# Kernel optimization log

Measured on AMD Instinct MI355X. Metric: run time of the kernel, lower is better.

Reference implementation:

```python
import jax, jax.numpy as jnp
import numpy as np

B, T, H, L, V = 256, 20, 512, 2, 8964
LQ, LH, LI = 40, 80, 49
BETA = 3.0


def setup_inputs() -> dict:
    key = jax.random.key(0)
    ks = iter(jax.random.split(key, 40))
    s = 1.0 / np.sqrt(H)
    n = lambda shape, sc=s: jax.random.normal(next(ks), shape, jnp.float32) * sc
    inp = {
        'emb': n((B, T, H), 1.0),
        'question': n((B, LQ, 2 * H), 1.0),
        'history': n((B, LH, 2 * H), 1.0),
        'image': n((B, LI, 2 * H), 1.0),
        'h0': jnp.zeros((L, B, H), jnp.float32),
        'c0': jnp.zeros((L, B, H), jnp.float32),
        # LSTM params (both layers have input dim H since ninp == nhid)
        'Wih': n((L, 4 * H, H)), 'Whh': n((L, 4 * H, H)),
        'bih': jnp.zeros((L, 4 * H), jnp.float32), 'bhh': jnp.zeros((L, 4 * H), jnp.float32),
        # question attention: w_q (2H->H), ans_q (H->H), Wa_q (H->1)
        'Wq': n((H, 2 * H)), 'bq': jnp.zeros((H,), jnp.float32),
        'Wansq': n((H, H)), 'bansq': jnp.zeros((H,), jnp.float32),
        'waq': n((1, H)), 'baq': jnp.zeros((1,), jnp.float32),
        # history attention
        'Wh': n((H, 2 * H)), 'bh': jnp.zeros((H,), jnp.float32),
        'Wansh': n((H, H)), 'bansh': jnp.zeros((H,), jnp.float32),
        'wah': n((1, H)), 'bah': jnp.zeros((1,), jnp.float32),
        # image attention
        'Wi': n((H, 2 * H)), 'bi': jnp.zeros((H,), jnp.float32),
        'Wansi': n((H, H)), 'bansi': jnp.zeros((H,), jnp.float32),
        'wai': n((1, H)), 'bai': jnp.zeros((1,), jnp.float32),
        # concat fusion (3H -> H)
        'Wcat': n((H, 3 * H)), 'bcat': jnp.zeros((H,), jnp.float32),
        # decoder SimpleClassifier: 2H -> 4H -> V
        'Wd1': n((4 * H, 2 * H)), 'bd1': jnp.zeros((4 * H,), jnp.float32),
        'Wd2': n((V, 4 * H), 1.0 / np.sqrt(4 * H)), 'bd2': jnp.zeros((V,), jnp.float32),
    }
    return inp


def reference(emb, question, history, image, h0, c0,
              Wih, Whh, bih, bhh,
              Wq, bq, Wansq, bansq, waq, baq,
              Wh, bh, Wansh, bansh, wah, bah,
              Wi, bi, Wansi, bansi, wai, bai,
              Wcat, bcat, Wd1, bd1, Wd2, bd2):
    nlayers = Wih.shape[0]
    # context projections are timestep-invariant: hoist out of the loop
    q_emb = question @ Wq.T + bq   # [B, LQ, H]
    h_emb = history @ Wh.T + bh    # [B, LH, H]
    i_emb = image @ Wi.T + bi      # [B, LI, H]

    def attend(ctx, out, Wans, bans, wa, ba):
        # ctx: [B, Lx, H], out: [B, H]
        a = jnp.tanh(ctx + (out @ Wans.T + bans)[:, None, :])
        logits = jnp.einsum('blh,h->bl', a, wa[0]) + ba[0]
        w = jax.nn.softmax(logits, axis=1)
        return jnp.einsum('bl,blh->bh', w, ctx)

    def step(carry, x_t):
        h, c = carry  # each [L, B, H]
        inp = x_t
        hs, cs = [], []
        for l in range(nlayers):
            gates = inp @ Wih[l].T + h[l] @ Whh[l].T + bih[l] + bhh[l]
            gi, gf, gg, go = jnp.split(gates, 4, axis=-1)  # torch gate order i,f,g,o
            cn = jax.nn.sigmoid(gf) * c[l] + jax.nn.sigmoid(gi) * jnp.tanh(gg)
            hn = jax.nn.sigmoid(go) * jnp.tanh(cn)
            hs.append(hn); cs.append(cn)
            inp = hn
        out = inp  # top-layer output [B, H]
        fq = attend(q_emb, out, Wansq, bansq, waq, baq)
        fh = attend(h_emb, out, Wansh, bansh, wah, bah)
        fi = attend(i_emb, out, Wansi, bansi, wai, bai)
        cat = jnp.tanh(jnp.concatenate([fq, fh, fi], axis=1) @ Wcat.T + bcat)
        fusion = jnp.concatenate([out, cat], axis=1)  # [B, 2H]
        dec = jax.nn.relu(fusion @ Wd1.T + bd1) @ Wd2.T + bd2
        lp = jax.nn.log_softmax(BETA * dec, axis=1)
        return (jnp.stack(hs), jnp.stack(cs)), lp

    (hT, cT), lps = jax.lax.scan(step, (h0, c0), jnp.swapaxes(emb, 0, 1))
    return jnp.swapaxes(lps, 0, 1), hT, cT
```

## Files before the change

### kernel.cpp

```cpp
#include <hip/hip_runtime.h>
#include <cmath>

#define B_ 256
#define T_ 20
#define H_ 512
#define V_ 8964
#define LQ_ 40
#define LH_ 80
#define LI_ 49
#define BT_ (B_ * T_)
#define BH_ (B_ * H_)
#define NPAD_ 9216
#define BETA_ 3.0f

#define MEGA_LSTM_ 128
#define MEGA_CTXQ_ 320
#define MEGA_CTXH_ 640
#define MEGA_CTXI_ 392
#define MEGA_CTX_ (MEGA_CTXQ_ + MEGA_CTXH_ + MEGA_CTXI_)
#define MEGA_GRID_ (MEGA_LSTM_ + MEGA_CTX_)

#define PREP_WCVT_ 2560
#define PREP_WD2_  9216
#define PREP_EMB_  1280
#define PREP_PERM_ 2048
#define PREP_H0_   128
#define PREP_BIAS_ 2
#define PREP_GRID_ (PREP_WCVT_ + PREP_WD2_ + PREP_EMB_ + PREP_PERM_ + PREP_H0_ + PREP_BIAS_)

typedef __attribute__((ext_vector_type(8))) short bf16x8;
typedef __attribute__((ext_vector_type(4))) float f32x4;
typedef __attribute__((ext_vector_type(8))) unsigned short u16x8;

static __device__ __forceinline__ unsigned short f2bf(float f) {
    union { float f; unsigned u; } v; v.f = f;
    unsigned r = v.u + 0x7FFF + ((v.u >> 16) & 1);
    return (unsigned short)(r >> 16);
}
static __device__ __forceinline__ float bf2f(unsigned short u) {
    union { unsigned u; float f; } v; v.u = ((unsigned)u) << 16;
    return v.f;
}
static __device__ __forceinline__ float fast_tanh(float x) {
    const float e = __expf(2.f * x);
    return 1.f - 2.f * __builtin_amdgcn_rcpf(e + 1.f);
}
static __device__ __forceinline__ float fast_sigmoid(float x) {
    return __builtin_amdgcn_rcpf(1.f + __expf(-x));
}
static __device__ __forceinline__ void st16_sc(unsigned short* p, unsigned short v) {
    unsigned int vv = v;
    asm volatile("global_store_short %0, %1, off sc0 sc1" :: "v"(p), "v"(vv) : "memory");
}
static __device__ __forceinline__ int ld32_sc(const int* p) {
    int v;
    asm volatile("global_load_dword %0, %1, off sc0 sc1\n\t"
                 "s_waitcnt vmcnt(0)"
                 : "=v"(v) : "v"(p) : "memory");
    return v;
}
#define GLD16(g, l) __builtin_amdgcn_global_load_lds(                                   \
    (const __attribute__((address_space(1))) unsigned int*)(unsigned long long)(const void*)(g), \
    (__attribute__((address_space(3))) unsigned int*)(unsigned int)(unsigned long long)(void*)(l), \
    16, 0, 0)

static __device__ __forceinline__ u16x8 cvt8(const float* p)
{
    float4 a = *reinterpret_cast<const float4*>(p);
    float4 b = *reinterpret_cast<const float4*>(p + 4);
    u16x8 v;
    v[0] = f2bf(a.x); v[1] = f2bf(a.y); v[2] = f2bf(a.z); v[3] = f2bf(a.w);
    v[4] = f2bf(b.x); v[5] = f2bf(b.y); v[6] = f2bf(b.z); v[7] = f2bf(b.w);
    return v;
}

struct PrepArgs {
    const float* wsrc[8]; unsigned short* wdst[8];
    const float* Wd2; unsigned short* Wd2p;
    const float* emb; unsigned short* emb_bf;
    const float* psrc[4]; unsigned short* pdst[4];
    const float* h0; unsigned short* hbuf;
    const float* bih; const float* bhh; float* bp0; float* bp1;
};

__global__ __launch_bounds__(256) void prep_kernel(PrepArgs a)
{
    static constexpr long long WSZ[8] = {524288, 524288, 524288, 262144,
                                         262144, 262144, 786432, 2097152};
    int g = blockIdx.x;
    const int tid = threadIdx.x;

    if (g < PREP_WCVT_) {
        long long off = (long long)g * 2048;
        int seg = 0;
#pragma unroll
        for (int i = 0; i < 8; ++i)
            if (seg == i && off >= WSZ[i]) { off -= WSZ[i]; ++seg; }
        const long long e = off + (long long)tid * 8;
        *reinterpret_cast<u16x8*>(a.wdst[seg] + e) = cvt8(a.wsrc[seg] + e);
        return;
    }
    g -= PREP_WCVT_;
    if (g < PREP_WD2_) {
        const long long e = (long long)g * 2048 + tid * 8;
        const long long row = e >> 11;
        u16x8 v;
        if (row < V_) v = cvt8(a.Wd2 + e);
        else v = (u16x8)0;
        *reinterpret_cast<u16x8*>(a.Wd2p + e) = v;
        return;
    }
    g -= PREP_WD2_;
    if (g < PREP_EMB_) {
        const long long e = (long long)g * 2048 + tid * 8;
        *reinterpret_cast<u16x8*>(a.emb_bf + e) = cvt8(a.emb + e);
        return;
    }
    g -= PREP_EMB_;
    if (g < PREP_PERM_) {
        const int which = g >> 9;
        const long long e0 = ((long long)(g & 511) * 256 + tid) * 8;
        const int drow = (int)(e0 >> 9);
        const int col = (int)(e0 & 511);
        const int gg = (drow >> 4) & 3;
        const int hsrc = ((drow >> 6) << 4) | (drow & 15);
        const int srow = (gg << 9) | hsrc;
        *reinterpret_cast<u16x8*>(a.pdst[which] + e0) =
            cvt8(a.psrc[which] + (long long)srow * 512 + col);
        return;
    }
    g -= PREP_PERM_;
    if (g < PREP_H0_) {
        const int half = g >> 6;
        const long long e = (long long)(g & 63) * 2048 + tid * 8;
        unsigned short* dst = a.hbuf + (half ? 4LL * BH_ : 0LL);
        *reinterpret_cast<u16x8*>(dst + e) = cvt8(a.h0 + (long long)half * BH_ + e);
        return;
    }
    g -= PREP_H0_;
    {
        const float* b1 = g ? a.bih + 2048 : a.bih;
        const float* b2 = g ? a.bhh + 2048 : a.bhh;
        float* dst = g ? a.bp1 : a.bp0;
#pragma unroll
        for (int i = 0; i < 8; ++i) {
            const int n = i * 256 + tid;
            const int gg = (n >> 4) & 3;
            const int h = ((n >> 6) << 4) | (n & 15);
            const int orig = (gg << 9) | h;
            dst[n] = b1[orig] + b2[orig];
        }
    }
}

static __device__ __forceinline__ int4 ldA8f(const float* A, long long idx)
{
    union { int4 i4; u16x8 v; } r;
    r.v = cvt8(A + idx);
    return r.i4;
}

template <int ACT, int OUTBF, int AF32>
__global__ __launch_bounds__(256, 2) void mfma_gemm(
    const void* __restrict__ A, const unsigned short* __restrict__ W,
    const float* __restrict__ bias1, const float* __restrict__ bias2,
    void* __restrict__ C, long long ldc, int Nreal, int K)
{
    __shared__ __align__(16) unsigned short As[2][128][32];
    __shared__ __align__(16) unsigned short Bs[2][128][32];
    const int tid = threadIdx.x;
    const int lane = tid & 63;
    const int wave = tid >> 6;
    const int wm = wave >> 1, wn = wave & 1;

    const int nwg = gridDim.x * gridDim.y;
    const int orig = blockIdx.y * gridDim.x + blockIdx.x;
    const int xcd = orig & 7, base = orig >> 3;
    const int q8 = nwg >> 3, r8 = nwg & 7;
    const int wg = (xcd < r8 ? xcd * (q8 + 1) : r8 * (q8 + 1) + (xcd - r8) * q8) + base;

    int MI = 8192 / (K << AF32);
    if (MI < 1) MI = 1;
    if (MI > (int)gridDim.y) MI = gridDim.y;
    const int slabSz = gridDim.x * MI;
    const int fullSlabs = gridDim.y / MI;
    const int fullRegion = fullSlabs * slabSz;
    int m0, n0;
    if (wg < fullRegion) {
        const int mb = wg / slabSz, rem = wg % slabSz;
        m0 = (mb * MI + rem % MI) * 128;
        n0 = (rem / MI) * 128;
    } else {
        const int rem = wg - fullRegion;
        const int TM = gridDim.y - fullSlabs * MI;
        m0 = (fullSlabs * MI + rem % TM) * 128;
        n0 = (rem / TM) * 128;
    }

    const int r = tid >> 2;
    const int ck = (tid & 3) * 8;

    const unsigned short* Wp = W + (long long)n0 * K;

    f32x4 acc[4][4] = {};
    int cur = 0;

    if constexpr (!AF32) {
        const unsigned short* Ab = (const unsigned short*)A;
        auto issue = [&](int k0, int buf) {
            const unsigned short* ga0 = Ab + (long long)(m0 + r) * K + k0 + ck;
            const unsigned short* ga1 = Ab + (long long)(m0 + r + 64) * K + k0 + ck;
            const unsigned short* gb0 = Wp + (long long)r * K + k0 + ck;
            const unsigned short* gb1 = Wp + (long long)(r + 64) * K + k0 + ck;
            char* lA = (char*)&As[buf][0][0] + wave * 1024;
            char* lB = (char*)&Bs[buf][0][0] + wave * 1024;
            GLD16(ga0, lA);
            GLD16(ga1, lA + 4096);
            GLD16(gb0, lB);
            GLD16(gb1, lB + 4096);
        };
        issue(0, 0);
        for (int k0 = 0; k0 < K; k0 += 32, cur ^= 1) {
            __syncthreads();
            if (k0 + 32 < K) issue(k0 + 32, cur ^ 1);
            const int lr = lane & 15, lk = (lane >> 4) * 8;
            bf16x8 af[4], bfr[4];
#pragma unroll
            for (int i = 0; i < 4; ++i) {
                af[i]  = *reinterpret_cast<const bf16x8*>(&As[cur][wm * 64 + i * 16 + lr][lk]);
                bfr[i] = *reinterpret_cast<const bf16x8*>(&Bs[cur][wn * 64 + i * 16 + lr][lk]);
            }
#pragma unroll
            for (int i = 0; i < 4; ++i)
#pragma unroll
                for (int j = 0; j < 4; ++j)
                    acc[i][j] = __builtin_amdgcn_mfma_f32_16x16x32_bf16(
                        af[i], bfr[j], acc[i][j], 0, 0, 0);
        }
    } else {
        const float* Af = (const float*)A;
        int4 ra0, ra1, rb0, rb1;
        ra0 = ldA8f(Af, (long long)(m0 + r) * K + ck);
        ra1 = ldA8f(Af, (long long)(m0 + r + 64) * K + ck);
        rb0 = *reinterpret_cast<const int4*>(Wp + (long long)r * K + ck);
        rb1 = *reinterpret_cast<const int4*>(Wp + (long long)(r + 64) * K + ck);
        for (int k0 = 0; k0 < K; k0 += 32, cur ^= 1) {
            *reinterpret_cast<int4*>(&As[cur][r][ck]) = ra0;
            *reinterpret_cast<int4*>(&As[cur][r + 64][ck]) = ra1;
            *reinterpret_cast<int4*>(&Bs[cur][r][ck]) = rb0;
            *reinterpret_cast<int4*>(&Bs[cur][r + 64][ck]) = rb1;
            __syncthreads();
            if (k0 + 32 < K) {
                const int kn = k0 + 32 + ck;
                ra0 = ldA8f(Af, (long long)(m0 + r) * K + kn);
                ra1 = ldA8f(Af, (long long)(m0 + r + 64) * K + kn);
                rb0 = *reinterpret_cast<const int4*>(Wp + (long long)r * K + kn);
                rb1 = *reinterpret_cast<const int4*>(Wp + (long long)(r + 64) * K + kn);
            }
            const int lr = lane & 15, lk = (lane >> 4) * 8;
            bf16x8 af[4], bfr[4];
#pragma unroll
            for (int i = 0; i < 4; ++i) {
                af[i]  = *reinterpret_cast<const bf16x8*>(&As[cur][wm * 64 + i * 16 + lr][lk]);
                bfr[i] = *reinterpret_cast<const bf16x8*>(&Bs[cur][wn * 64 + i * 16 + lr][lk]);
            }
#pragma unroll
            for (int i = 0; i < 4; ++i)
#pragma unroll
                for (int j = 0; j < 4; ++j)
                    acc[i][j] = __builtin_amdgcn_mfma_f32_16x16x32_bf16(
                        af[i], bfr[j], acc[i][j], 0, 0, 0);
        }
    }

    const int lr = lane & 15, lrow4 = (lane >> 4) * 4;
#pragma unroll
    for (int j = 0; j < 4; ++j) {
        const int col = n0 + wn * 64 + j * 16 + lr;
        if (col >= Nreal) continue;
        float bsum = 0.f;
        if (bias1) bsum += bias1[col];
        if (bias2) bsum += bias2[col];
#pragma unroll
        for (int i = 0; i < 4; ++i) {
#pragma unroll
            for (int rr = 0; rr < 4; ++rr) {
                const int row = m0 + wm * 64 + i * 16 + lrow4 + rr;
                float v = acc[i][j][rr] + bsum;
                if (ACT == 1) v = fast_tanh(v);
                if (ACT == 2) v = fmaxf(v, 0.f);
                if (OUTBF)
                    ((unsigned short*)C)[(long long)row * ldc + col] = f2bf(v);
                else
                    ((float*)C)[(long long)row * ldc + col] = v;
            }
        }
    }
}

static void mgemm(hipStream_t s, int act, int outbf, int af32,
                  const void* A, const unsigned short* W,
                  const float* b1, const float* b2,
                  void* C, long long ldc, int M, int Nreal, int K)
{
    dim3 grid((Nreal + 127) / 128, M / 128), blk(256);
#define MG(a, o, f) mfma_gemm<a, o, f><<<grid, blk, 0, s>>>(A, W, b1, b2, C, ldc, Nreal, K)
    if (af32) {
        if (outbf) { if (act == 1) MG(1,1,1); else if (act == 2) MG(2,1,1); else MG(0,1,1); }
        else       { if (act == 1) MG(1,0,1); else if (act == 2) MG(2,0,1); else MG(0,0,1); }
    } else {
        if (outbf) { if (act == 1) MG(1,1,0); else if (act == 2) MG(2,1,0); else MG(0,1,0); }
        else       { if (act == 1) MG(1,0,0); else if (act == 2) MG(2,0,0); else MG(0,0,0); }
    }
#undef MG
}

__global__ __launch_bounds__(512, 1) void gemm256_kernel(
    const unsigned short* __restrict__ A, const unsigned short* __restrict__ W,
    const float* __restrict__ bias, float* __restrict__ C)
{
    __shared__ __align__(16) unsigned short As[2][256][64];
    __shared__ __align__(16) unsigned short Bs[2][256][64];
    const int tid = threadIdx.x;
    const int lane = tid & 63;
    const int wave = tid >> 6;
    const int wm = wave >> 2, wn = wave & 3;
    const int lr = lane & 15, hi = lane >> 4;
    const int K = 2048;

    const int nwg = gridDim.x * gridDim.y;
    const int orig = blockIdx.y * gridDim.x + blockIdx.x;
    const int xcd = orig & 7, base = orig >> 3;
    const int q8 = nwg >> 3, r8 = nwg & 7;
    const int wg = (xcd < r8 ? xcd * (q8 + 1) : r8 * (q8 + 1) + (xcd - r8) * q8) + base;
    const int MI = 2;
    const int slabSz = gridDim.x * MI;
    int m0, n0;
    {
        const int mb = wg / slabSz, rem = wg % slabSz;
        m0 = (mb * MI + rem % MI) * 256;
        n0 = (rem / MI) * 256;
    }

    const int srow = lane >> 3;
    const int scol = ((lane & 7) ^ srow) * 8;
    auto stage = [&](int kt, int b) {
#pragma unroll
        for (int q = 0; q < 4; ++q) {
            const int c = wave * 4 + q;
            const unsigned short* ga = A + (long long)(m0 + 8 * c + srow) * K + kt * 64 + scol;
            GLD16(ga, (char*)&As[b][0][0] + c * 1024);
        }
#pragma unroll
        for (int q = 0; q < 4; ++q) {
            const int c = wave * 4 + q;
            const unsigned short* gw = W + (long long)(n0 + 8 * c + srow) * K + kt * 64 + scol;
            GLD16(gw, (char*)&Bs[b][0][0] + c * 1024);
        }
    };

    f32x4 acc[8][4] = {};
    const int nt = K / 64;
    const int cx = ((lr & 7) * 8);
    stage(0, 0);
    stage(1, 1);

    for (int t = 0; t < nt; ++t) {
        const int b = t & 1;
        if (t + 1 < nt) asm volatile("s_waitcnt vmcnt(8)" ::: "memory");
        else            asm volatile("s_waitcnt vmcnt(0)" ::: "memory");
        __builtin_amdgcn_s_barrier();

#pragma unroll
        for (int p = 0; p < 3; ++p) {
            const int mh = p & 1, ks = p >> 1;
            const int col = (ks * 32 + hi * 8) ^ cx;
            bf16x8 af[4], bfr[4];
#pragma unroll
            for (int i = 0; i < 4; ++i) {
                af[i]  = *reinterpret_cast<const bf16x8*>(
                    &As[b][wm * 128 + mh * 64 + i * 16 + lr][col]);
                bfr[i] = *reinterpret_cast<const bf16x8*>(
                    &Bs[b][wn * 64 + i * 16 + lr][col]);
            }
            __builtin_amdgcn_s_setprio(1);
#pragma unroll
            for (int i = 0; i < 4; ++i)
#pragma unroll
                for (int j = 0; j < 4; ++j)
                    acc[mh * 4 + i][j] = __builtin_amdgcn_mfma_f32_16x16x32_bf16(
                        af[i], bfr[j], acc[mh * 4 + i][j], 0, 0, 0);
            __builtin_amdgcn_s_setprio(0);
            __builtin_amdgcn_s_barrier();
        }
        {
            const int col = (32 + hi * 8) ^ cx;
            bf16x8 af[4], bfr[4];
#pragma unroll
            for (int i = 0; i < 4; ++i) {
                af[i]  = *reinterpret_cast<const bf16x8*>(
                    &As[b][wm * 128 + 64 + i * 16 + lr][col]);
                bfr[i] = *reinterpret_cast<const bf16x8*>(
                    &Bs[b][wn * 64 + i * 16 + lr][col]);
            }
            asm volatile("s_waitcnt lgkmcnt(0)" ::: "memory");
            __builtin_amdgcn_sched_barrier(0);
            __builtin_amdgcn_s_barrier();
            if (t + 2 < nt) stage(t + 2, b);
            __builtin_amdgcn_s_setprio(1);
#pragma unroll
            for (int i = 0; i < 4; ++i)
#pragma unroll
                for (int j = 0; j < 4; ++j)
                    acc[4 + i][j] = __builtin_amdgcn_mfma_f32_16x16x32_bf16(
                        af[i], bfr[j], acc[4 + i][j], 0, 0, 0);
            __builtin_amdgcn_s_setprio(0);
        }
    }

#pragma unroll
    for (int j = 0; j < 4; ++j) {
        const int col = n0 + wn * 64 + j * 16 + lr;
        if (col >= V_) continue;
        const float bsum = bias[col];
#pragma unroll
        for (int i8 = 0; i8 < 8; ++i8) {
#pragma unroll
            for (int rr = 0; rr < 4; ++rr) {
                const int row = m0 + wm * 128 + i8 * 16 + hi * 4 + rr;
                C[(long long)row * V_ + col] = acc[i8][j][rr] + bsum;
            }
        }
    }
}

#define LSTM_ISSUE(b_, dst_) do {                                              \
    const unsigned short* pa_ = (((b_) >> 2) ? q20 : q10) + ((b_) & 3) * 128;  \
    const unsigned short* pb_ = (((b_) >> 2) ? q21 : q11) + ((b_) & 3) * 128;  \
    asm volatile(                                                              \
        "global_load_dwordx4 %0, %[pa], off sc0 sc1\n\t"                       \
        "global_load_dwordx4 %1, %[pa], off offset:64 sc0 sc1\n\t"             \
        "global_load_dwordx4 %2, %[pa], off offset:128 sc0 sc1\n\t"            \
        "global_load_dwordx4 %3, %[pa], off offset:192 sc0 sc1\n\t"            \
        "global_load_dwordx4 %4, %[pb], off sc0 sc1\n\t"                       \
        "global_load_dwordx4 %5, %[pb], off offset:64 sc0 sc1\n\t"             \
        "global_load_dwordx4 %6, %[pb], off offset:128 sc0 sc1\n\t"            \
        "global_load_dwordx4 %7, %[pb], off offset:192 sc0 sc1"                \
        : "=&v"((dst_)[0]), "=&v"((dst_)[1]), "=&v"((dst_)[2]), "=&v"((dst_)[3]), \
          "=&v"((dst_)[4]), "=&v"((dst_)[5]), "=&v"((dst_)[6]), "=&v"((dst_)[7])  \
        : [pa] "v"(pa_), [pb] "v"(pb_)                                         \
        : "memory");                                                           \
} while (0)

__global__ __launch_bounds__(256, 1) void mega_kernel(
    const unsigned short* __restrict__ emb_bf,
    const unsigned short* __restrict__ Wih0p, const unsigned short* __restrict__ Whh0p,
    const unsigned short* __restrict__ Wih1p, const unsigned short* __restrict__ Whh1p,
    const float* __restrict__ bp0, const float* __restrict__ bp1,
    const float* __restrict__ c0,
    unsigned short* __restrict__ hbuf,
    float* __restrict__ st_h, float* __restrict__ st_c,
    unsigned short* __restrict__ h_top,
    int* flags,
    const float* __restrict__ question, const float* __restrict__ history,
    const float* __restrict__ image,
    const unsigned short* __restrict__ Wq_bf, const unsigned short* __restrict__ Wh_bf,
    const unsigned short* __restrict__ Wi_bf,
    const float* __restrict__ bq, const float* __restrict__ bhb,
    const float* __restrict__ bi,
    unsigned short* __restrict__ q_emb, unsigned short* __restrict__ h_emb,
    unsigned short* __restrict__ i_emb)
{
    __shared__ __align__(16) char smem[131072];
    const int gid = blockIdx.x;
    const int tid = threadIdx.x;

    if (gid >= MEGA_LSTM_) {
        int g = gid - MEGA_LSTM_;
        const float* A; const unsigned short* W; const float* bias;
        unsigned short* Cc;
        if (g < MEGA_CTXQ_)       { A = question; W = Wq_bf; bias = bq;  Cc = q_emb; }
        else if (g < MEGA_CTXQ_ + MEGA_CTXH_) {
            g -= MEGA_CTXQ_;        A = history;  W = Wh_bf; bias = bhb; Cc = h_emb; }
        else { g -= MEGA_CTXQ_ + MEGA_CTXH_; A = image; W = Wi_bf; bias = bi; Cc = i_emb; }
        const int m0 = (g >> 2) * 128, n0 = (g & 3) * 128;
        const int K = 1024;

        unsigned short (*As)[128][32] = (unsigned short (*)[128][32])smem;
        unsigned short (*Bs)[128][32] = (unsigned short (*)[128][32])(smem + 16384);
        const int lane = tid & 63;
        const int wave = tid >> 6;
        const int wm = wave >> 1, wn = wave & 1;
        const int r = tid >> 2;
        const int ck = (tid & 3) * 8;
        const unsigned short* Wp = W + (long long)n0 * K;

        f32x4 acc[4][4] = {};
        int4 ra0, ra1, rb0, rb1;
        ra0 = ldA8f(A, (long long)(m0 + r) * K + ck);
        ra1 = ldA8f(A, (long long)(m0 + r + 64) * K + ck);
        rb0 = *reinterpret_cast<const int4*>(Wp + (long long)r * K + ck);
        rb1 = *reinterpret_cast<const int4*>(Wp + (long long)(r + 64) * K + ck);
        int cur = 0;
        for (int k0 = 0; k0 < K; k0 += 32, cur ^= 1) {
            *reinterpret_cast<int4*>(&As[cur][r][ck]) = ra0;
            *reinterpret_cast<int4*>(&As[cur][r + 64][ck]) = ra1;
            *reinterpret_cast<int4*>(&Bs[cur][r][ck]) = rb0;
            *reinterpret_cast<int4*>(&Bs[cur][r + 64][ck]) = rb1;
            __syncthreads();
            if (k0 + 32 < K) {
                const int kn = k0 + 32 + ck;
                ra0 = ldA8f(A, (long long)(m0 + r) * K + kn);
                ra1 = ldA8f(A, (long long)(m0 + r + 64) * K + kn);
                rb0 = *reinterpret_cast<const int4*>(Wp + (long long)r * K + kn);
                rb1 = *reinterpret_cast<const int4*>(Wp + (long long)(r + 64) * K + kn);
            }
            const int lr = lane & 15, lk = (lane >> 4) * 8;
            bf16x8 af[4], bfr[4];
#pragma unroll
            for (int i = 0; i < 4; ++i) {
                af[i]  = *reinterpret_cast<const bf16x8*>(&As[cur][wm * 64 + i * 16 + lr][lk]);
                bfr[i] = *reinterpret_cast<const bf16x8*>(&Bs[cur][wn * 64 + i * 16 + lr][lk]);
            }
#pragma unroll
            for (int i = 0; i < 4; ++i)
#pragma unroll
                for (int j = 0; j < 4; ++j)
                    acc[i][j] = __builtin_amdgcn_mfma_f32_16x16x32_bf16(
                        af[i], bfr[j], acc[i][j], 0, 0, 0);
        }
        const int lr = lane & 15, lrow4 = (lane >> 4) * 4;
#pragma unroll
        for (int j = 0; j < 4; ++j) {
            const int col = n0 + wn * 64 + j * 16 + lr;
            const float bsum = bias[col];
#pragma unroll
            for (int i = 0; i < 4; ++i)
#pragma unroll
                for (int rr = 0; rr < 4; ++rr) {
                    const int row = m0 + wm * 64 + i * 16 + lrow4 + rr;
                    Cc[(long long)row * 512 + col] = f2bf(acc[i][j][rr] + bsum);
                }
        }
        return;
    }

    const int grp = gid >> 6;
    const int id  = gid & 63;
    const int mt = id >> 5, nt = id & 31;
    const int m0 = mt * 128, n0 = nt * 64;
    const int lane = tid & 63;
    const int w = tid >> 6;
    const int lr = lane & 15;
    const int hi = lane >> 4;
    const int hi4 = hi * 4;

    const unsigned short* W1g = (grp ? Wih1p : Wih0p) + (long long)n0 * H_;
    const unsigned short* W2g = (grp ? Whh1p : Whh0p) + (long long)n0 * H_;

#pragma unroll
    for (int it = 0; it < 16; ++it) {
        const int e = (tid + it * 256) * 8;
        const int row = e >> 9, col = e & 511;
        const int bir = (col * 2) ^ ((row & 7) << 4);
        char* dst = smem + row * 1024 + bir;
        *reinterpret_cast<int4*>(dst) =
            *reinterpret_cast<const int4*>(W1g + (long long)row * H_ + col);
        *reinterpret_cast<int4*>(dst + 65536) =
            *reinterpret_cast<const int4*>(W2g + (long long)row * H_ + col);
    }
    __syncthreads();

    const int h = nt * 16 + lr;
    const float* bp = grp ? bp1 : bp0;
    float bg[4];
#pragma unroll
    for (int g = 0; g < 4; ++g) bg[g] = bp[n0 + g * 16 + lr];

    const int ar0 = m0 + w * 32 + lr;
    const int ar1 = ar0 + 16;

    float cregA[4], cregB[4], hn0[4], hn1[4];
#pragma unroll
    for (int rr = 0; rr < 4; ++rr) {
        cregA[rr] = c0[(long long)grp * BH_ + (long long)(m0 + w * 32 + hi4 + rr) * H_ + h];
        cregB[rr] = c0[(long long)grp * BH_ + (long long)(m0 + w * 32 + 16 + hi4 + rr) * H_ + h];
    }

    int bbase[4];
#pragma unroll
    for (int j = 0; j < 4; ++j)
        bbase[j] = (j * 16 + lr) * 1024 + ((hi * 16) ^ ((lr & 3) << 4));
    const int xk6 = ((lr >> 2) & 1) << 6;

    int* myFlag = flags + (mt * 64 + grp * 32 + nt) * 16;
    const long long sEmb = (long long)T_ * H_;

    for (int s = 0; s <= T_; ++s) {
        const bool active = (grp == 0) ? (s < T_) : (s >= 1);
        const int t = grp ? (s - 1) : s;
        if (active) {
            const unsigned short *A1, *A2;
            long long sA1;
            unsigned short* hout;
            if (grp == 0) {
                A1 = emb_bf + (long long)t * H_; sA1 = sEmb;
                A2 = hbuf + (long long)(s % 3) * BH_;
                hout = hbuf + (long long)((s + 1) % 3) * BH_;
            } else {
                A1 = hbuf + (long long)(s % 3) * BH_; sA1 = H_;
                A2 = hbuf + (long long)(3 + (s & 1)) * BH_;
                hout = hbuf + (long long)(3 + ((s + 1) & 1)) * BH_;
            }
            const unsigned short* q10 = A1 + (long long)ar0 * sA1 + hi * 8;
            const unsigned short* q11 = A1 + (long long)ar1 * sA1 + hi * 8;
            const unsigned short* q20 = A2 + (long long)ar0 * H_ + hi * 8;
            const unsigned short* q21 = A2 + (long long)ar1 * H_ + hi * 8;

            int4 buf[3][8];
            LSTM_ISSUE(0, buf[0]);
            LSTM_ISSUE(1, buf[1]);
            LSTM_ISSUE(2, buf[2]);

            f32x4 accA[4] = {}, accB[4] = {};
#pragma unroll
            for (int b = 0; b < 8; ++b) {
                if (b < 6)      asm volatile("s_waitcnt vmcnt(16)" ::: "memory");
                else if (b == 6) asm volatile("s_waitcnt vmcnt(8)" ::: "memory");
                else             asm volatile("s_waitcnt vmcnt(0)" ::: "memory");
                __builtin_amdgcn_sched_barrier(0);
#pragma unroll
                for (int i = 0; i < 4; ++i) {
                    const int it = b * 4 + i;
                    const int kk = it & 15, p = it >> 4;
                    const bf16x8 a0 = *reinterpret_cast<const bf16x8*>(&buf[b % 3][i]);
                    const bf16x8 a1 = *reinterpret_cast<const bf16x8*>(&buf[b % 3][4 + i]);
                    const int kb = ((kk << 6) ^ xk6) + (p << 16);
#pragma unroll
                    for (int j = 0; j < 4; ++j) {
                        const bf16x8 bfv = *reinterpret_cast<const bf16x8*>(
                            smem + bbase[j] + kb);
                        accA[j] = __builtin_amdgcn_mfma_f32_16x16x32_bf16(a0, bfv, accA[j], 0, 0, 0);
                        accB[j] = __builtin_amdgcn_mfma_f32_16x16x32_bf16(a1, bfv, accB[j], 0, 0, 0);
                    }
                }
                if (b + 3 < 8) LSTM_ISSUE(b + 3, buf[b % 3]);
            }

#pragma unroll
            for (int rr = 0; rr < 4; ++rr) {
                {
                    const int b = m0 + w * 32 + hi4 + rr;
                    const float i_ = fast_sigmoid(accA[0][rr] + bg[0]);
                    const float f_ = fast_sigmoid(accA[1][rr] + bg[1]);
                    const float g_ = fast_tanh(accA[2][rr] + bg[2]);
                    const float o_ = fast_sigmoid(accA[3][rr] + bg[3]);
                    const float cn = f_ * cregA[rr] + i_ * g_;
                    const float hn = o_ * fast_tanh(cn);
                    cregA[rr] = cn; hn0[rr] = hn;
                    st16_sc(&hout[(long long)b * H_ + h], f2bf(hn));
                }
                {
                    const int b = m0 + w * 32 + 16 + hi4 + rr;
                    const float i_ = fast_sigmoid(accB[0][rr] + bg[0]);
                    const float f_ = fast_sigmoid(accB[1][rr] + bg[1]);
                    const float g_ = fast_tanh(accB[2][rr] + bg[2]);
                    const float o_ = fast_sigmoid(accB[3][rr] + bg[3]);
                    const float cn = f_ * cregB[rr] + i_ * g_;
                    const float hn = o_ * fast_tanh(cn);
                    cregB[rr] = cn; hn1[rr] = hn;
                    st16_sc(&hout[(long long)b * H_ + h], f2bf(hn));
                }
            }
            if (s == T_) {
#pragma unroll
                for (int rr = 0; rr < 4; ++rr) {
                    const int b0r = m0 + w * 32 + hi4 + rr;
                    const int b1r = b0r + 16;
                    h_top[((long long)b0r * T_ + t) * H_ + h] = f2bf(hn0[rr]);
                    h_top[((long long)b1r * T_ + t) * H_ + h] = f2bf(hn1[rr]);
                    st_h[(long long)grp * BH_ + (long long)b0r * H_ + h] = hn0[rr];
                    st_h[(long long)grp * BH_ + (long long)b1r * H_ + h] = hn1[rr];
                    st_c[(long long)grp * BH_ + (long long)b0r * H_ + h] = cregA[rr];
                    st_c[(long long)grp * BH_ + (long long)b1r * H_ + h] = cregB[rr];
                }
            }
        }
        if (s < T_) {
            __syncthreads();
            if (tid == 0) {
                int v = s + 1;
                asm volatile("global_store_dword %0, %1, off sc0 sc1"
                             :: "v"(myFlag), "v"(v) : "memory");
            }
            if (active) {
#pragma unroll
                for (int rr = 0; rr < 4; ++rr) {
                    const int b0r = m0 + w * 32 + hi4 + rr;
                    const int b1r = b0r + 16;
                    if (grp == 1) {
                        h_top[((long long)b0r * T_ + t) * H_ + h] = f2bf(hn0[rr]);
                        h_top[((long long)b1r * T_ + t) * H_ + h] = f2bf(hn1[rr]);
                    }
                    if (t == T_ - 1) {
                        st_h[(long long)grp * BH_ + (long long)b0r * H_ + h] = hn0[rr];
                        st_h[(long long)grp * BH_ + (long long)b1r * H_ + h] = hn1[rr];
                        st_c[(long long)grp * BH_ + (long long)b0r * H_ + h] = cregA[rr];
                        st_c[(long long)grp * BH_ + (long long)b1r * H_ + h] = cregB[rr];
                    }
                }
            }
            if (tid < 64) {
                const int thr = (grp == 0 && tid >= 32) ? s : s + 1;
                const int* fp = flags + (mt * 64 + tid) * 16;
                while (ld32_sc(fp) < thr) __builtin_amdgcn_s_sleep(2);
            }
            __syncthreads();
        }
    }
}

__global__ __launch_bounds__(256) void attend3_kernel(
    const unsigned short* __restrict__ q_emb, const unsigned short* __restrict__ h_emb,
    const unsigned short* __restrict__ i_emb,
    const float* __restrict__ proj3,
    const float* __restrict__ waq, const float* __restrict__ baq, const float* __restrict__ bansq,
    const float* __restrict__ wah, const float* __restrict__ bah, const float* __restrict__ bansh,
    const float* __restrict__ wai, const float* __restrict__ bai, const float* __restrict__ bansi,
    const unsigned short* __restrict__ h_top,
    unsigned short* __restrict__ fcat, unsigned short* __restrict__ fusion)
{
    __shared__ float p_lds[512];
    __shared__ float wa_lds[512];
    __shared__ float lg[96];
    const int bt0 = blockIdx.x;
    const int bt = (bt0 & 7) * (BT_ / 8) + (bt0 >> 3);
    const int c = blockIdx.y;
    const int b = bt / T_;
    const int tid = threadIdx.x;
    const int wid = tid >> 6, lane = tid & 63;

    if (c == 0 && tid < 64)
        *reinterpret_cast<u16x8*>(&fusion[(long long)bt * 1024 + tid * 8]) =
            *reinterpret_cast<const u16x8*>(&h_top[(long long)bt * 512 + tid * 8]);

    const unsigned short* ctx = c == 0 ? q_emb : c == 1 ? h_emb : i_emb;
    const int Lx = c == 0 ? LQ_ : c == 1 ? LH_ : LI_;
    const float* wa = c == 0 ? waq : c == 1 ? wah : wai;
    const float bav = (c == 0 ? baq : c == 1 ? bah : bai)[0];
    const float* bans = c == 0 ? bansq : c == 1 ? bansh : bansi;

    p_lds[tid]       = proj3[(long long)bt * 1536 + c * 512 + tid] + bans[tid];
    p_lds[tid + 256] = proj3[(long long)bt * 1536 + c * 512 + tid + 256] + bans[tid + 256];
    wa_lds[tid] = wa[tid];
    wa_lds[tid + 256] = wa[tid + 256];
    __syncthreads();

    for (int l = wid; l < Lx; l += 4) {
        const unsigned short* crow = ctx + ((long long)b * Lx + l) * H_;
        float acc = 0.f;
#pragma unroll
        for (int j = 0; j < 8; ++j) {
            const int hp = lane + 64 * j;
            acc += wa_lds[hp] * fast_tanh(bf2f(crow[hp]) + p_lds[hp]);
        }
        for (int o = 32; o > 0; o >>= 1) acc += __shfl_down(acc, o);
        if (lane == 0) lg[l] = acc + bav;
    }
    __syncthreads();
    if (tid == 0) {
        float m = -1e30f;
        for (int l = 0; l < Lx; ++l) m = fmaxf(m, lg[l]);
        float ssum = 0.f;
        for (int l = 0; l < Lx; ++l) { const float e = __expf(lg[l] - m); lg[l] = e; ssum += e; }
        const float inv = __builtin_amdgcn_rcpf(ssum);
        for (int l = 0; l < Lx; ++l) lg[l] *= inv;
    }
    __syncthreads();
    for (int hp = tid; hp < H_; hp += 256) {
        float acc = 0.f;
        for (int l = 0; l < Lx; ++l)
            acc += lg[l] * bf2f(ctx[((long long)b * Lx + l) * H_ + hp]);
        fcat[(long long)bt * 1536 + c * 512 + hp] = f2bf(acc);
    }
}

__global__ __launch_bounds__(256) void log_softmax_kernel(float* __restrict__ out)
{
    __shared__ float red[4];
    __shared__ float bc;
    const long long base = (long long)blockIdx.x * V_;
    const int tid = threadIdx.x, lane = tid & 63, wid = tid >> 6;

    float r[36];
    float m = -1e30f;
#pragma unroll
    for (int i = 0; i < 36; ++i) {
        const int v = tid + i * 256;
        r[i] = (v < V_) ? BETA_ * out[base + v] : -1e30f;
        m = fmaxf(m, r[i]);
    }
    for (int o = 32; o > 0; o >>= 1) m = fmaxf(m, __shfl_down(m, o));
    if (lane == 0) red[wid] = m;
    __syncthreads();
    if (tid == 0)
        bc = fmaxf(fmaxf(red[0], red[1]), fmaxf(red[2], red[3]));
    __syncthreads();
    m = bc;

    float s = 0.f;
#pragma unroll
    for (int i = 0; i < 36; ++i) s += __expf(r[i] - m);
    for (int o = 32; o > 0; o >>= 1) s += __shfl_down(s, o);
    if (lane == 0) red[wid] = s;
    __syncthreads();
    if (tid == 0) bc = m + logf(red[0] + red[1] + red[2] + red[3]);
    __syncthreads();
    const float ls = bc;
#pragma unroll
    for (int i = 0; i < 36; ++i) {
        const int v = tid + i * 256;
        if (v < V_) out[base + v] = r[i] - ls;
    }
}

extern "C" void kernel_launch(void* const* d_in, const int* in_sizes, int n_in,
                              void* d_out_, int out_size, void* d_ws, size_t ws_size,
                              hipStream_t stream)
{
    const float* emb      = (const float*)d_in[0];
    const float* question = (const float*)d_in[1];
    const float* history  = (const float*)d_in[2];
    const float* image    = (const float*)d_in[3];
    const float* h0       = (const float*)d_in[4];
    const float* c0       = (const float*)d_in[5];
    const float* Wih      = (const float*)d_in[6];
    const float* Whh      = (const float*)d_in[7];
    const float* bih      = (const float*)d_in[8];
    const float* bhh      = (const float*)d_in[9];
    const float* Wq    = (const float*)d_in[10]; const float* bq    = (const float*)d_in[11];
    const float* Wansq = (const float*)d_in[12]; const float* bansq = (const float*)d_in[13];
    const float* waq   = (const float*)d_in[14]; const float* baq   = (const float*)d_in[15];
    const float* Wh    = (const float*)d_in[16]; const float* bh    = (const float*)d_in[17];
    const float* Wansh = (const float*)d_in[18]; const float* bansh = (const float*)d_in[19];
    const float* wah   = (const float*)d_in[20]; const float* bah   = (const float*)d_in[21];
    const float* Wi    = (const float*)d_in[22]; const float* bi    = (const float*)d_in[23];
    const float* Wansi = (const float*)d_in[24]; const float* bansi = (const float*)d_in[25];
    const float* wai   = (const float*)d_in[26]; const float* bai   = (const float*)d_in[27];
    const float* Wcat  = (const float*)d_in[28]; const float* bcat  = (const float*)d_in[29];
    const float* Wd1   = (const float*)d_in[30]; const float* bd1   = (const float*)d_in[31];
    const float* Wd2   = (const float*)d_in[32]; const float* bd2   = (const float*)d_in[33];

    float* out = (float*)d_out_;

    int*   flags = (int*)d_ws;
    float* st_h = (float*)((char*)d_ws + 8192);
    float* st_c = st_h + 2LL * BH_;
    float* bp0  = st_c + 2LL * BH_;
    float* bp1  = bp0 + 2048;
    unsigned short* hbuf   = (unsigned short*)(bp1 + 2048);
    unsigned short* Wih0p  = hbuf + 5LL * BH_;
    unsigned short* Whh0p  = Wih0p + 2048LL * H_;
    unsigned short* Wih1p  = Whh0p + 2048LL * H_;
    unsigned short* Whh1p  = Wih1p + 2048LL * H_;
    unsigned short* emb_bf = Whh1p + 2048LL * H_;
    unsigned short* h_top_bf = emb_bf + (long long)BT_ * H_;
    unsigned short* q_emb_bf = h_top_bf + (long long)BT_ * H_;
    unsigned short* h_emb_bf = q_emb_bf + (long long)B_ * LQ_ * H_;
    unsigned short* i_emb_bf = h_emb_bf + (long long)B_ * LH_ * H_;
    unsigned short* dec1_bf  = i_emb_bf + (long long)B_ * LI_ * H_;
    unsigned short* Wd2p_bf  = dec1_bf + (long long)BT_ * 4 * H_;

    unsigned short* Wq_bf    = (unsigned short*)out;
    unsigned short* Wh_bf    = Wq_bf + 524288;
    unsigned short* Wi_bf    = Wh_bf + 524288;
    unsigned short* Wansq_bf = Wi_bf + 524288;
    unsigned short* Wansh_bf = Wansq_bf + 262144;
    unsigned short* Wansi_bf = Wansh_bf + 262144;
    unsigned short* Wcat_bf  = Wansi_bf + 262144;
    unsigned short* Wd1_bf   = Wcat_bf + 786432;
    float* proj3 = (float*)(Wd1_bf + 2097152);
    unsigned short* fcat_bf   = (unsigned short*)(proj3 + (long long)BT_ * 1536);
    unsigned short* fusion_bf = fcat_bf + (long long)BT_ * 1536;

    {
        PrepArgs a;
        a.wsrc[0] = Wq;    a.wdst[0] = Wq_bf;
        a.wsrc[1] = Wh;    a.wdst[1] = Wh_bf;
        a.wsrc[2] = Wi;    a.wdst[2] = Wi_bf;
        a.wsrc[3] = Wansq; a.wdst[3] = Wansq_bf;
        a.wsrc[4] = Wansh; a.wdst[4] = Wansh_bf;
        a.wsrc[5] = Wansi; a.wdst[5] = Wansi_bf;
        a.wsrc[6] = Wcat;  a.wdst[6] = Wcat_bf;
        a.wsrc[7] = Wd1;   a.wdst[7] = Wd1_bf;
        a.Wd2 = Wd2; a.Wd2p = Wd2p_bf;
        a.emb = emb; a.emb_bf = emb_bf;
        a.psrc[0] = Wih;               a.pdst[0] = Wih0p;
        a.psrc[1] = Whh;               a.pdst[1] = Whh0p;
        a.psrc[2] = Wih + 2048LL * H_; a.pdst[2] = Wih1p;
        a.psrc[3] = Whh + 2048LL * H_; a.pdst[3] = Whh1p;
        a.h0 = h0; a.hbuf = hbuf;
        a.bih = bih; a.bhh = bhh; a.bp0 = bp0; a.bp1 = bp1;
        prep_kernel<<<dim3(PREP_GRID_), dim3(256), 0, stream>>>(a);
    }
    hipMemsetAsync(flags, 0, 8192, stream);

    mega_kernel<<<dim3(MEGA_GRID_), dim3(256), 0, stream>>>(
        emb_bf, Wih0p, Whh0p, Wih1p, Whh1p, bp0, bp1, c0,
        hbuf, st_h, st_c, h_top_bf, flags,
        question, history, image, Wq_bf, Wh_bf, Wi_bf, bq, bh, bi,
        q_emb_bf, h_emb_bf, i_emb_bf);

    mgemm(stream, 0, 0, 0, h_top_bf, Wansq_bf, nullptr, nullptr, proj3, 1536, BT_, 1536, H_);
    attend3_kernel<<<dim3(BT_, 3), dim3(256), 0, stream>>>(
        q_emb_bf, h_emb_bf, i_emb_bf, proj3,
        waq, baq, bansq, wah, bah, bansh, wai, bai, bansi,
        h_top_bf, fcat_bf, fusion_bf);

    mgemm(stream, 1, 1, 0, fcat_bf, Wcat_bf, bcat, nullptr, fusion_bf + H_, 2 * H_, BT_, H_, 3 * H_);

    mgemm(stream, 2, 1, 0, fusion_bf, Wd1_bf, bd1, nullptr, dec1_bf, 4 * H_, BT_, 4 * H_, 2 * H_);
    gemm256_kernel<<<dim3(NPAD_ / 256, BT_ / 256), dim3(512), 0, stream>>>(
        dec1_bf, Wd2p_bf, bd2, out);

    log_softmax_kernel<<<dim3(BT_), dim3(256), 0, stream>>>(out);

    hipMemcpyAsync(out + (long long)BT_ * V_, st_h,
                   4LL * BH_ * sizeof(float), hipMemcpyDeviceToDevice, stream);
}
```

Measured before the change: 896.2 us.

## Merge LSTM batch tiles into 512-thread blocks, halving persistent LSTM workgroups

The persistent LSTM section now uses 64 workgroups of 512 threads, each covering the full batch of 256 instead of two 128-row batch tiles. This halves the number of blocks spinning on cross-block flags per timestep and shares each weight slice held in LDS across twice as many batch rows. The context-projection GEMM blocks also run at 512 threads with a smaller per-wave tile. The cost is fewer blocks to spread the recurrent work over, more waves per block contending on __syncthreads, and possible register pressure under launch_bounds(512,1).

Result: slower. 956.5 us (+6.7%).

```diff
diff --git a/kernel.cpp b/kernel.cpp
--- a/kernel.cpp
+++ b/kernel.cpp
@@ -13,7 +13,7 @@
 #define NPAD_ 9216
 #define BETA_ 3.0f
 
-#define MEGA_LSTM_ 128
+#define MEGA_LSTM_ 64
 #define MEGA_CTXQ_ 320
 #define MEGA_CTXH_ 640
 #define MEGA_CTXI_ 392
@@ -452,7 +452,7 @@
         : "memory");                                                           \
 } while (0)
 
-__global__ __launch_bounds__(256, 1) void mega_kernel(
+__global__ __launch_bounds__(512, 1) void mega_kernel(
     const unsigned short* __restrict__ emb_bf,
     const unsigned short* __restrict__ Wih0p, const unsigned short* __restrict__ Whh0p,
     const unsigned short* __restrict__ Wih1p, const unsigned short* __restrict__ Whh1p,
@@ -490,40 +490,37 @@
         unsigned short (*Bs)[128][32] = (unsigned short (*)[128][32])(smem + 16384);
         const int lane = tid & 63;
         const int wave = tid >> 6;
-        const int wm = wave >> 1, wn = wave & 1;
+        const int wm4 = wave >> 1, wn2 = wave & 1;
         const int r = tid >> 2;
         const int ck = (tid & 3) * 8;
         const unsigned short* Wp = W + (long long)n0 * K;
 
-        f32x4 acc[4][4] = {};
-        int4 ra0, ra1, rb0, rb1;
+        f32x4 acc[2][4] = {};
+        int4 ra0, rb0;
         ra0 = ldA8f(A, (long long)(m0 + r) * K + ck);
-        ra1 = ldA8f(A, (long long)(m0 + r + 64) * K + ck);
         rb0 = *reinterpret_cast<const int4*>(Wp + (long long)r * K + ck);
-        rb1 = *reinterpret_cast<const int4*>(Wp + (long long)(r + 64) * K + ck);
         int cur = 0;
         for (int k0 = 0; k0 < K; k0 += 32, cur ^= 1) {
             *reinterpret_cast<int4*>(&As[cur][r][ck]) = ra0;
-            *reinterpret_cast<int4*>(&As[cur][r + 64][ck]) = ra1;
             *reinterpret_cast<int4*>(&Bs[cur][r][ck]) = rb0;
-            *reinterpret_cast<int4*>(&Bs[cur][r + 64][ck]) = rb1;
             __syncthreads();
             if (k0 + 32 < K) {
                 const int kn = k0 + 32 + ck;
                 ra0 = ldA8f(A, (long long)(m0 + r) * K + kn);
-                ra1 = ldA8f(A, (long long)(m0 + r + 64) * K + kn);
                 rb0 = *reinterpret_cast<const int4*>(Wp + (long long)r * K + kn);
-                rb1 = *reinterpret_cast<const int4*>(Wp + (long long)(r + 64) * K + kn);
             }
             const int lr = lane & 15, lk = (lane >> 4) * 8;
-            bf16x8 af[4], bfr[4];
-#pragma unroll
-            for (int i = 0; i < 4; ++i) {
-                af[i]  = *reinterpret_cast<const bf16x8*>(&As[cur][wm * 64 + i * 16 + lr][lk]);
-                bfr[i] = *reinterpret_cast<const bf16x8*>(&Bs[cur][wn * 64 + i * 16 + lr][lk]);
-            }
-#pragma unroll
-            for (int i = 0; i < 4; ++i)
+            bf16x8 af[2], bfr[4];
+#pragma unroll
+            for (int i = 0; i < 2; ++i)
+                af[i] = *reinterpret_cast<const bf16x8*>(
+                    &As[cur][wm4 * 32 + i * 16 + lr][lk]);
+#pragma unroll
+            for (int j = 0; j < 4; ++j)
+                bfr[j] = *reinterpret_cast<const bf16x8*>(
+                    &Bs[cur][wn2 * 64 + j * 16 + lr][lk]);
+#pragma unroll
+            for (int i = 0; i < 2; ++i)
 #pragma unroll
                 for (int j = 0; j < 4; ++j)
                     acc[i][j] = __builtin_amdgcn_mfma_f32_16x16x32_bf16(
@@ -532,23 +529,22 @@
         const int lr = lane & 15, lrow4 = (lane >> 4) * 4;
 #pragma unroll
         for (int j = 0; j < 4; ++j) {
-            const int col = n0 + wn * 64 + j * 16 + lr;
+            const int col = n0 + wn2 * 64 + j * 16 + lr;
             const float bsum = bias[col];
 #pragma unroll
-            for (int i = 0; i < 4; ++i)
+            for (int i = 0; i < 2; ++i)
 #pragma unroll
                 for (int rr = 0; rr < 4; ++rr) {
-                    const int row = m0 + wm * 64 + i * 16 + lrow4 + rr;
+                    const int row = m0 + wm4 * 32 + i * 16 + lrow4 + rr;
                     Cc[(long long)row * 512 + col] = f2bf(acc[i][j][rr] + bsum);
                 }
         }
         return;
     }
 
-    const int grp = gid >> 6;
-    const int id  = gid & 63;
-    const int mt = id >> 5, nt = id & 31;
-    const int m0 = mt * 128, n0 = nt * 64;
+    const int grp = gid >> 5;
+    const int nt  = gid & 31;
+    const int n0 = nt * 64;
     const int lane = tid & 63;
     const int w = tid >> 6;
     const int lr = lane & 15;
@@ -559,8 +555,8 @@
     const unsigned short* W2g = (grp ? Whh1p : Whh0p) + (long long)n0 * H_;
 
 #pragma unroll
-    for (int it = 0; it < 16; ++it) {
-        const int e = (tid + it * 256) * 8;
+    for (int it = 0; it < 8; ++it) {
+        const int e = (tid + it * 512) * 8;
         const int row = e >> 9, col = e & 511;
         const int bir = (col * 2) ^ ((row & 7) << 4);
         char* dst = smem + row * 1024 + bir;
@@ -577,23 +573,23 @@
 #pragma unroll
     for (int g = 0; g < 4; ++g) bg[g] = bp[n0 + g * 16 + lr];
 
-    const int ar0 = m0 + w * 32 + lr;
+    const int ar0 = w * 32 + lr;
     const int ar1 = ar0 + 16;
 
     float cregA[4], cregB[4], hn0[4], hn1[4];
 #pragma unroll
     for (int rr = 0; rr < 4; ++rr) {
-        cregA[rr] = c0[(long long)grp * BH_ + (long long)(m0 + w * 32 + hi4 + rr) * H_ + h];
-        cregB[rr] = c0[(long long)grp * BH_ + (long long)(m0 + w * 32 + 16 + hi4 + rr) * H_ + h];
-    }
-
+        cregA[rr] = c0[(long long)grp * BH_ + (long long)(w * 32 + hi4 + rr) * H_ + h];
+        cregB[rr] = c0[(long long)grp * BH_ + (long long)(w * 32 + 16 + hi4 + rr) * H_ + h];
+    }
+
+    const int xk6 = ((lr >> 2) & 1) << 6;
     int bbase[4];
 #pragma unroll
     for (int j = 0; j < 4; ++j)
         bbase[j] = (j * 16 + lr) * 1024 + ((hi * 16) ^ ((lr & 3) << 4));
-    const int xk6 = ((lr >> 2) & 1) << 6;
-
-    int* myFlag = flags + (mt * 64 + grp * 32 + nt) * 16;
+
+    int* myFlag = flags + (grp * 32 + nt) * 16;
     const long long sEmb = (long long)T_ * H_;
 
     for (int s = 0; s <= T_; ++s) {
@@ -650,7 +646,7 @@
 #pragma unroll
             for (int rr = 0; rr < 4; ++rr) {
                 {
-                    const int b = m0 + w * 32 + hi4 + rr;
+                    const int b = w * 32 + hi4 + rr;
                     const float i_ = fast_sigmoid(accA[0][rr] + bg[0]);
                     const float f_ = fast_sigmoid(accA[1][rr] + bg[1]);
                     const float g_ = fast_tanh(accA[2][rr] + bg[2]);
@@ -661,7 +657,7 @@
                     st16_sc(&hout[(long long)b * H_ + h], f2bf(hn));
                 }
                 {
-                    const int b = m0 + w * 32 + 16 + hi4 + rr;
+                    const int b = w * 32 + 16 + hi4 + rr;
                     const float i_ = fast_sigmoid(accB[0][rr] + bg[0]);
                     const float f_ = fast_sigmoid(accB[1][rr] + bg[1]);
                     const float g_ = fast_tanh(accB[2][rr] + bg[2]);
@@ -675,7 +671,7 @@
             if (s == T_) {
 #pragma unroll
                 for (int rr = 0; rr < 4; ++rr) {
-                    const int b0r = m0 + w * 32 + hi4 + rr;
+                    const int b0r = w * 32 + hi4 + rr;
                     const int b1r = b0r + 16;
                     h_top[((long long)b0r * T_ + t) * H_ + h] = f2bf(hn0[rr]);
                     h_top[((long long)b1r * T_ + t) * H_ + h] = f2bf(hn1[rr]);
@@ -696,7 +692,7 @@
             if (active) {
 #pragma unroll
                 for (int rr = 0; rr < 4; ++rr) {
-                    const int b0r = m0 + w * 32 + hi4 + rr;
+                    const int b0r = w * 32 + hi4 + rr;
                     const int b1r = b0r + 16;
                     if (grp == 1) {
                         h_top[((long long)b0r * T_ + t) * H_ + h] = f2bf(hn0[rr]);
@@ -712,7 +708,7 @@
             }
             if (tid < 64) {
                 const int thr = (grp == 0 && tid >= 32) ? s : s + 1;
-                const int* fp = flags + (mt * 64 + tid) * 16;
+                const int* fp = flags + tid * 16;
                 while (ld32_sc(fp) < thr) __builtin_amdgcn_s_sleep(2);
             }
             __syncthreads();
@@ -905,7 +901,7 @@
     }
     hipMemsetAsync(flags, 0, 8192, stream);
 
-    mega_kernel<<<dim3(MEGA_GRID_), dim3(256), 0, stream>>>(
+    mega_kernel<<<dim3(MEGA_GRID_), dim3(512), 0, stream>>>(
         emb_bf, Wih0p, Whh0p, Wih1p, Whh1p, bp0, bp1, c0,
         hbuf, st_h, st_c, h_top_bf, flags,
         question, history, image, Wq_bf, Wh_bf, Wi_bf, bq, bh, bi,
```

## Move late-use weight conversions into mega kernel to overlap with LSTM

Applied to the files above, without the earlier changes.

Weight conversions that are only needed after the recurrent stage (Wd2 padding, Wans*, Wcat, Wd1) move out of the prep kernel and into extra blocks appended to the mega kernel grid. They can then run concurrently with the latency-bound LSTM recurrence instead of serialising before it. The prep kernel shrinks to the conversions the mega kernel itself needs. The risk is that the extra conversion blocks compete for CUs or memory bandwidth with the LSTM blocks, which spin on flags and depend on co-residency.

New measurement: 902.9 us. Within noise of the previous version (+0.8%).

```diff
diff --git a/kernel.cpp b/kernel.cpp
--- a/kernel.cpp
+++ b/kernel.cpp
@@ -18,15 +18,16 @@
 #define MEGA_CTXH_ 640
 #define MEGA_CTXI_ 392
 #define MEGA_CTX_ (MEGA_CTXQ_ + MEGA_CTXH_ + MEGA_CTXI_)
-#define MEGA_GRID_ (MEGA_LSTM_ + MEGA_CTX_)
-
-#define PREP_WCVT_ 2560
-#define PREP_WD2_  9216
+#define MEGA_WD2_ 1152
+#define MEGA_CVT_ 224
+#define MEGA_GRID_ (MEGA_LSTM_ + MEGA_CTX_ + MEGA_WD2_ + MEGA_CVT_)
+
+#define PREP_WCVT_ 768
 #define PREP_EMB_  1280
 #define PREP_PERM_ 2048
 #define PREP_H0_   128
 #define PREP_BIAS_ 2
-#define PREP_GRID_ (PREP_WCVT_ + PREP_WD2_ + PREP_EMB_ + PREP_PERM_ + PREP_H0_ + PREP_BIAS_)
+#define PREP_GRID_ (PREP_WCVT_ + PREP_EMB_ + PREP_PERM_ + PREP_H0_ + PREP_BIAS_)
 
 typedef __attribute__((ext_vector_type(8))) short bf16x8;
 typedef __attribute__((ext_vector_type(4))) float f32x4;
@@ -75,8 +76,7 @@
 }
 
 struct PrepArgs {
-    const float* wsrc[8]; unsigned short* wdst[8];
-    const float* Wd2; unsigned short* Wd2p;
+    const float* wsrc[3]; unsigned short* wdst[3];
     const float* emb; unsigned short* emb_bf;
     const float* psrc[4]; unsigned short* pdst[4];
     const float* h0; unsigned short* hbuf;
@@ -85,32 +85,16 @@
 
 __global__ __launch_bounds__(256) void prep_kernel(PrepArgs a)
 {
-    static constexpr long long WSZ[8] = {524288, 524288, 524288, 262144,
-                                         262144, 262144, 786432, 2097152};
     int g = blockIdx.x;
     const int tid = threadIdx.x;
 
     if (g < PREP_WCVT_) {
-        long long off = (long long)g * 2048;
-        int seg = 0;
-#pragma unroll
-        for (int i = 0; i < 8; ++i)
-            if (seg == i && off >= WSZ[i]) { off -= WSZ[i]; ++seg; }
-        const long long e = off + (long long)tid * 8;
+        const int seg = g >> 8;
+        const long long e = (long long)(g & 255) * 2048 + tid * 8;
         *reinterpret_cast<u16x8*>(a.wdst[seg] + e) = cvt8(a.wsrc[seg] + e);
         return;
     }
     g -= PREP_WCVT_;
-    if (g < PREP_WD2_) {
-        const long long e = (long long)g * 2048 + tid * 8;
-        const long long row = e >> 11;
-        u16x8 v;
-        if (row < V_) v = cvt8(a.Wd2 + e);
-        else v = (u16x8)0;
-        *reinterpret_cast<u16x8*>(a.Wd2p + e) = v;
-        return;
-    }
-    g -= PREP_WD2_;
     if (g < PREP_EMB_) {
         const long long e = (long long)g * 2048 + tid * 8;
         *reinterpret_cast<u16x8*>(a.emb_bf + e) = cvt8(a.emb + e);
@@ -434,6 +418,11 @@
     }
 }
 
+struct CvtArgs {
+    const float* Wd2; unsigned short* Wd2p;
+    const float* wsrc[5]; unsigned short* wdst[5];
+};
+
 #define LSTM_ISSUE(b_, dst_) do {                                              \
     const unsigned short* pa_ = (((b_) >> 2) ? q20 : q10) + ((b_) & 3) * 128;  \
     const unsigned short* pb_ = (((b_) >> 2) ? q21 : q11) + ((b_) & 3) * 128;  \
@@ -469,11 +458,43 @@
     const float* __restrict__ bq, const float* __restrict__ bhb,
     const float* __restrict__ bi,
     unsigned short* __restrict__ q_emb, unsigned short* __restrict__ h_emb,
-    unsigned short* __restrict__ i_emb)
+    unsigned short* __restrict__ i_emb,
+    CvtArgs cv)
 {
     __shared__ __align__(16) char smem[131072];
     const int gid = blockIdx.x;
     const int tid = threadIdx.x;
+
+    if (gid >= MEGA_LSTM_ + MEGA_CTX_) {
+        int cg = gid - (MEGA_LSTM_ + MEGA_CTX_);
+        if (cg < MEGA_WD2_) {
+            const long long base = (long long)cg * 16384;
+#pragma unroll
+            for (int it = 0; it < 8; ++it) {
+                const long long e = base + it * 2048 + tid * 8;
+                const long long row = e >> 11;
+                u16x8 v;
+                if (row < V_) v = cvt8(cv.Wd2 + e);
+                else v = (u16x8)0;
+                *reinterpret_cast<u16x8*>(cv.Wd2p + e) = v;
+            }
+        } else {
+            cg -= MEGA_WD2_;
+            static constexpr long long WSZ[5] = {262144, 262144, 262144,
+                                                 786432, 2097152};
+            long long off = (long long)cg * 16384;
+            int seg = 0;
+#pragma unroll
+            for (int i = 0; i < 5; ++i)
+                if (seg == i && off >= WSZ[i]) { off -= WSZ[i]; ++seg; }
+#pragma unroll
+            for (int it = 0; it < 8; ++it) {
+                const long long e = off + it * 2048 + tid * 8;
+                *reinterpret_cast<u16x8*>(cv.wdst[seg] + e) = cvt8(cv.wsrc[seg] + e);
+            }
+        }
+        return;
+    }
 
     if (gid >= MEGA_LSTM_) {
         int g = gid - MEGA_LSTM_;
@@ -885,15 +906,9 @@
 
     {
         PrepArgs a;
-        a.wsrc[0] = Wq;    a.wdst[0] = Wq_bf;
-        a.wsrc[1] = Wh;    a.wdst[1] = Wh_bf;
-        a.wsrc[2] = Wi;    a.wdst[2] = Wi_bf;
-        a.wsrc[3] = Wansq; a.wdst[3] = Wansq_bf;
-        a.wsrc[4] = Wansh; a.wdst[4] = Wansh_bf;
-        a.wsrc[5] = Wansi; a.wdst[5] = Wansi_bf;
-        a.wsrc[6] = Wcat;  a.wdst[6] = Wcat_bf;
-        a.wsrc[7] = Wd1;   a.wdst[7] = Wd1_bf;
-        a.Wd2 = Wd2; a.Wd2p = Wd2p_bf;
+        a.wsrc[0] = Wq; a.wdst[0] = Wq_bf;
+        a.wsrc[1] = Wh; a.wdst[1] = Wh_bf;
+        a.wsrc[2] = Wi; a.wdst[2] = Wi_bf;
         a.emb = emb; a.emb_bf = emb_bf;
         a.psrc[0] = Wih;               a.pdst[0] = Wih0p;
         a.psrc[1] = Whh;               a.pdst[1] = Whh0p;
@@ -905,11 +920,20 @@
     }
     hipMemsetAsync(flags, 0, 8192, stream);
 
-    mega_kernel<<<dim3(MEGA_GRID_), dim3(256), 0, stream>>>(
-        emb_bf, Wih0p, Whh0p, Wih1p, Whh1p, bp0, bp1, c0,
-        hbuf, st_h, st_c, h_top_bf, flags,
-        question, history, image, Wq_bf, Wh_bf, Wi_bf, bq, bh, bi,
-        q_emb_bf, h_emb_bf, i_emb_bf);
+    {
+        CvtArgs cv;
+        cv.Wd2 = Wd2; cv.Wd2p = Wd2p_bf;
+        cv.wsrc[0] = Wansq; cv.wdst[0] = Wansq_bf;
+        cv.wsrc[1] = Wansh; cv.wdst[1] = Wansh_bf;
+        cv.wsrc[2] = Wansi; cv.wdst[2] = Wansi_bf;
+        cv.wsrc[3] = Wcat;  cv.wdst[3] = Wcat_bf;
+        cv.wsrc[4] = Wd1;   cv.wdst[4] = Wd1_bf;
+        mega_kernel<<<dim3(MEGA_GRID_), dim3(256), 0, stream>>>(
+            emb_bf, Wih0p, Whh0p, Wih1p, Whh1p, bp0, bp1, c0,
+            hbuf, st_h, st_c, h_top_bf, flags,
+            question, history, image, Wq_bf, Wh_bf, Wi_bf, bq, bh, bi,
+            q_emb_bf, h_emb_bf, i_emb_bf, cv);
+    }
 
     mgemm(stream, 0, 0, 0, h_top_bf, Wansq_bf, nullptr, nullptr, proj3, 1536, BT_, 1536, H_);
     attend3_kernel<<<dim3(BT_, 3), dim3(256), 0, stream>>>(
```
